# Kernel tuning notes

Hardware: AMD Instinct MI355X
Metric: run time of the kernel (lower is better)

The kernel has to match this reference:

```python
import jax, jax.numpy as jnp
import numpy as np

NEG_SLOPE = 0.01  # nn.LeakyReLU default


def setup_inputs() -> dict:
    key = jax.random.key(0)
    k1, k2, k3, k4, k5, k6 = jax.random.split(key, 6)
    N, E, F_IN, F_OUT = 50000, 800000, 256, 64
    x = jax.random.normal(k1, (N, F_IN), dtype=jnp.float32)
    src = jax.random.randint(k2, (E,), 0, N, dtype=jnp.int32)
    dst = jax.random.randint(k3, (E,), 0, N, dtype=jnp.int32)
    # nn.init.normal_(weight, 0, 0.5) for both Linear layers (no bias)
    W1 = 0.5 * jax.random.normal(k4, (F_OUT, F_IN), dtype=jnp.float32)
    W2 = 0.5 * jax.random.normal(k5, (F_OUT, F_OUT), dtype=jnp.float32)
    # detGAT.a = torch.rand(2*out_feats, 1)
    a = jax.random.uniform(k6, (2 * F_OUT, 1), dtype=jnp.float32)
    return {"x": x, "W1": W1, "W2": W2, "a": a, "src": src, "dst": dst}


def reference(x, W1, W2, a, src, dst):
    N, d = x.shape[0], W1.shape[0]
    # model_base: linear -> (dropout, identity in eval) -> relu, twice
    z = jax.nn.relu(x @ W1.T)
    h = jax.nn.relu(z @ W2.T)  # [N, d]
    # detGAT edge score: LeakyReLU(concat([h_dst, h_src]) @ a)
    # split a so we compute per-node dot products once instead of an [E, 2d] concat
    a_dst, a_src = a[:d, 0], a[d:, 0]
    s_dst = h @ a_dst  # [N]
    s_src = h @ a_src  # [N]
    score = jax.nn.leaky_relu(s_dst[dst] + s_src[src], NEG_SLOPE)  # [E]
    # edge_softmax: softmax over incoming edges of each destination node
    m = jax.ops.segment_max(score, dst, num_segments=N)  # [N]
    e = jnp.exp(score - m[dst])
    ssum = jax.ops.segment_sum(e, dst, num_segments=N)  # [N]
    w = e / ssum[dst]  # [E]
    # weighted scatter-sum of src features to dst nodes
    res = jax.ops.segment_sum(h[src] * w[:, None], dst, num_segments=N)  # [N, d]
    return jax.nn.relu(h - res)
```

## Files before the change

kernel.cpp:

```cpp
#include <hip/hip_runtime.h>
#include <math.h>

#define F_IN 256
#define F_OUT 64
#define NEG_SLOPE 0.01f
#define CAP 8192
#define NB2 256

typedef unsigned short ushort8_t __attribute__((ext_vector_type(8)));
typedef __bf16 bf16x8 __attribute__((ext_vector_type(8)));
typedef float f32x16 __attribute__((ext_vector_type(16)));

__device__ inline unsigned short f2bf(float f) {
    unsigned u = __float_as_uint(f);
    u += 0x7FFF + ((u >> 16) & 1);
    return (unsigned short)(u >> 16);
}
__device__ inline float bf2f(unsigned short u) {
    return __uint_as_float(((unsigned)u) << 16);
}
__device__ inline void splitbf(float x, unsigned short& hi, unsigned short& lo) {
    hi = f2bf(x);
    lo = f2bf(x - bf2f(hi));
}
__device__ inline bf16x8 asbf8(ushort8_t u) {
    union { ushort8_t u; bf16x8 b; } c; c.u = u; return c.b;
}
__device__ inline void split8(const float4& p0, const float4& p1, bf16x8& ah, bf16x8& al) {
    ushort8_t h, l;
    unsigned short th, tl;
    splitbf(p0.x, th, tl); h[0] = th; l[0] = tl;
    splitbf(p0.y, th, tl); h[1] = th; l[1] = tl;
    splitbf(p0.z, th, tl); h[2] = th; l[2] = tl;
    splitbf(p0.w, th, tl); h[3] = th; l[3] = tl;
    splitbf(p1.x, th, tl); h[4] = th; l[4] = tl;
    splitbf(p1.y, th, tl); h[5] = th; l[5] = tl;
    splitbf(p1.z, th, tl); h[6] = th; l[6] = tl;
    splitbf(p1.w, th, tl); h[7] = th; l[7] = tl;
    ah = asbf8(h); al = asbf8(l);
}
__device__ inline float redq32(float v) {
    v += __shfl_xor(v, 1);  v += __shfl_xor(v, 2);  v += __shfl_xor(v, 4);
    v += __shfl_xor(v, 8);  v += __shfl_xor(v, 16);
    return v;
}

__global__ __launch_bounds__(1024)
void prep_scatter_kernel(const float* __restrict__ W1, const float* __restrict__ W2,
                         unsigned short* __restrict__ w1fh, unsigned short* __restrict__ w1fl,
                         unsigned short* __restrict__ w2fh, unsigned short* __restrict__ w2fl,
                         const int* __restrict__ src, const int* __restrict__ dst,
                         int* __restrict__ cursor, int* __restrict__ edata,
                         int E, int chunk)
{
    __shared__ int lh[256], lbase[256], lcur[256];
    const int tid = threadIdx.x;

    if (blockIdx.x < 16) {
        int idx = blockIdx.x * 1024 + tid;
        int jj = idx & 7, l = (idx >> 3) & 63, t = idx >> 9;
        {
            int nt = t & 1, gks = t >> 1;
            int f = nt * 32 + (l & 31);
            int k = gks * 16 + (l >> 5) * 8 + jj;
            unsigned short hi, lo;
            splitbf(W1[f * F_IN + k], hi, lo);
            w1fh[idx] = hi; w1fl[idx] = lo;
        }
        if (idx < 4096) {
            int nt = t & 1, ks = t >> 1;
            int f = nt * 32 + (l & 31);
            int j = ks * 16 + (l >> 5) * 8 + jj;
            unsigned short hi, lo;
            splitbf(W2[f * F_OUT + j], hi, lo);
            w2fh[idx] = hi; w2fl[idx] = lo;
        }
        return;
    }

    const int bid = blockIdx.x - 16;
    if (tid < 256) lh[tid] = 0;
    __syncthreads();
    const int beg = bid * chunk;
    const int end = min(E, beg + chunk);
    for (int i = beg + tid; i < end; i += 1024)
        atomicAdd(&lh[((unsigned)dst[i]) >> 8], 1);
    __syncthreads();
    if (tid < 256) {
        int c = lh[tid];
        lbase[tid] = c ? atomicAdd(&cursor[tid], c) : 0;
        lcur[tid] = 0;
    }
    __syncthreads();
    for (int i = beg + tid; i < end; i += 1024) {
        int d = dst[i];
        int s = src[i];
        int b = ((unsigned)d) >> 8;
        int rk = atomicAdd(&lcur[b], 1);
        edata[b * CAP + lbase[b] + rk] = ((d & 0xFF) << 16) | s;
    }
}

__global__ __launch_bounds__(256)
void mlp_sort_kernel(const float* __restrict__ x,
                     const unsigned short* __restrict__ w1fh,
                     const unsigned short* __restrict__ w1fl,
                     const unsigned short* __restrict__ w2fh,
                     const unsigned short* __restrict__ w2fl,
                     const float* __restrict__ a,
                     unsigned short* __restrict__ hb,
                     float* __restrict__ sdst,
                     float* __restrict__ ssrc, int N,
                     const int* __restrict__ cursor,
                     const int* __restrict__ edata,
                     int* __restrict__ ssorted,
                     int* __restrict__ cnt, int* __restrict__ offs,
                     int MLPB)
{
    __shared__ __align__(16) unsigned short zbuf[4 * 4224];
    __shared__ int hist[256];
    __shared__ int excl[256];

    const int tid = threadIdx.x;
    const int lane = tid & 63;

    if (blockIdx.x < MLPB) {
        const int wid = __builtin_amdgcn_readfirstlane(tid >> 6);
        const int ml = lane & 31;
        const int q = lane >> 5;
        const int node0w = blockIdx.x * 128 + wid * 32;

        unsigned short* zh = zbuf + wid * 4224;
        unsigned short* zl = zh + 2112;

        const int rowc = min(node0w + ml, N - 1);
        const float* __restrict__ xrow = x + (size_t)rowc * F_IN + q * 8;

        f32x16 acc0, acc1;
#pragma unroll
        for (int i = 0; i < 16; i++) { acc0[i] = 0.f; acc1[i] = 0.f; }

        float4 p0 = *(const float4*)(xrow);
        float4 p1 = *(const float4*)(xrow + 4);
        ushort8_t b0h = *(const ushort8_t*)(w1fh + (lane) * 8);
        ushort8_t b0l = *(const ushort8_t*)(w1fl + (lane) * 8);
        ushort8_t b1h = *(const ushort8_t*)(w1fh + (64 + lane) * 8);
        ushort8_t b1l = *(const ushort8_t*)(w1fl + (64 + lane) * 8);

#pragma unroll
        for (int gks = 0; gks < 16; gks++) {
            const int nx = gks < 15 ? gks + 1 : 15;
            float4 q0 = *(const float4*)(xrow + nx * 16);
            float4 q1 = *(const float4*)(xrow + nx * 16 + 4);
            ushort8_t c0h = *(const ushort8_t*)(w1fh + ((nx * 2 + 0) * 64 + lane) * 8);
            ushort8_t c0l = *(const ushort8_t*)(w1fl + ((nx * 2 + 0) * 64 + lane) * 8);
            ushort8_t c1h = *(const ushort8_t*)(w1fh + ((nx * 2 + 1) * 64 + lane) * 8);
            ushort8_t c1l = *(const ushort8_t*)(w1fl + ((nx * 2 + 1) * 64 + lane) * 8);

            bf16x8 ah, al;
            split8(p0, p1, ah, al);
            acc0 = __builtin_amdgcn_mfma_f32_32x32x16_bf16(ah, asbf8(b0h), acc0, 0, 0, 0);
            acc0 = __builtin_amdgcn_mfma_f32_32x32x16_bf16(ah, asbf8(b0l), acc0, 0, 0, 0);
            acc0 = __builtin_amdgcn_mfma_f32_32x32x16_bf16(al, asbf8(b0h), acc0, 0, 0, 0);
            acc1 = __builtin_amdgcn_mfma_f32_32x32x16_bf16(ah, asbf8(b1h), acc1, 0, 0, 0);
            acc1 = __builtin_amdgcn_mfma_f32_32x32x16_bf16(ah, asbf8(b1l), acc1, 0, 0, 0);
            acc1 = __builtin_amdgcn_mfma_f32_32x32x16_bf16(al, asbf8(b1h), acc1, 0, 0, 0);

            p0 = q0; p1 = q1;
            b0h = c0h; b0l = c0l; b1h = c1h; b1l = c1l;
        }

#pragma unroll
        for (int reg = 0; reg < 16; reg++) {
            int nd = (reg & 3) + 8 * (reg >> 2) + 4 * q;
            float z0 = fmaxf(acc0[reg], 0.f);
            float z1 = fmaxf(acc1[reg], 0.f);
            unsigned short h_, l_;
            splitbf(z0, h_, l_);
            zh[nd * 66 + ml] = h_; zl[nd * 66 + ml] = l_;
            splitbf(z1, h_, l_);
            zh[nd * 66 + 32 + ml] = h_; zl[nd * 66 + 32 + ml] = l_;
        }

        f32x16 hacc0, hacc1;
#pragma unroll
        for (int i = 0; i < 16; i++) { hacc0[i] = 0.f; hacc1[i] = 0.f; }
#pragma unroll
        for (int ks = 0; ks < 4; ks++) {
            ushort8_t wh0 = *(const ushort8_t*)(w2fh + ((ks * 2 + 0) * 64 + lane) * 8);
            ushort8_t wl0 = *(const ushort8_t*)(w2fl + ((ks * 2 + 0) * 64 + lane) * 8);
            ushort8_t wh1 = *(const ushort8_t*)(w2fh + ((ks * 2 + 1) * 64 + lane) * 8);
            ushort8_t wl1 = *(const ushort8_t*)(w2fl + ((ks * 2 + 1) * 64 + lane) * 8);
            bf16x8 ah = asbf8(*(const ushort8_t*)(zh + ml * 66 + ks * 16 + q * 8));
            bf16x8 al = asbf8(*(const ushort8_t*)(zl + ml * 66 + ks * 16 + q * 8));
            hacc0 = __builtin_amdgcn_mfma_f32_32x32x16_bf16(ah, asbf8(wh0), hacc0, 0, 0, 0);
            hacc0 = __builtin_amdgcn_mfma_f32_32x32x16_bf16(ah, asbf8(wl0), hacc0, 0, 0, 0);
            hacc0 = __builtin_amdgcn_mfma_f32_32x32x16_bf16(al, asbf8(wh0), hacc0, 0, 0, 0);
            hacc1 = __builtin_amdgcn_mfma_f32_32x32x16_bf16(ah, asbf8(wh1), hacc1, 0, 0, 0);
            hacc1 = __builtin_amdgcn_mfma_f32_32x32x16_bf16(ah, asbf8(wl1), hacc1, 0, 0, 0);
            hacc1 = __builtin_amdgcn_mfma_f32_32x32x16_bf16(al, asbf8(wh1), hacc1, 0, 0, 0);
        }

        const float aD0 = a[ml],            aD1 = a[32 + ml];
        const float aS0 = a[F_OUT + ml],    aS1 = a[F_OUT + 32 + ml];

        float sdv = 0.f, ssv = 0.f;
#pragma unroll
        for (int reg = 0; reg < 16; reg++) {
            int nd = (reg & 3) + 8 * (reg >> 2) + 4 * q;
            float h0 = fmaxf(hacc0[reg], 0.f);
            float h1 = fmaxf(hacc1[reg], 0.f);
            float td = redq32(h0 * aD0 + h1 * aD1);
            float ts = redq32(h0 * aS0 + h1 * aS1);
            if (ml == nd) { sdv = td; ssv = ts; }
            int gn = node0w + nd;
            if (gn < N) {
                hb[(size_t)gn * F_OUT + ml]      = f2bf(h0);
                hb[(size_t)gn * F_OUT + 32 + ml] = f2bf(h1);
            }
        }
        {
            int gn = node0w + ml;
            if ((((ml >> 2) & 1) == q) && gn < N) {
                sdst[gn] = sdv;
                ssrc[gn] = ssv;
            }
        }
        return;
    }

    const int cb = blockIdx.x - MLPB;
    const int base = cb * CAP;
    const int ecnt = cursor[cb];

    hist[tid] = 0;
    __syncthreads();
    for (int i = tid; i < ecnt; i += 256)
        atomicAdd(&hist[((unsigned)edata[base + i]) >> 16], 1);
    __syncthreads();

    if (tid < 64) {
        int v0 = hist[lane * 4], v1 = hist[lane * 4 + 1];
        int v2 = hist[lane * 4 + 2], v3 = hist[lane * 4 + 3];
        int ts = v0 + v1 + v2 + v3;
        int s = ts;
#pragma unroll
        for (int d = 1; d < 64; d <<= 1) {
            int t = __shfl_up(s, d);
            if (lane >= d) s += t;
        }
        int e = s - ts;
        excl[lane * 4] = e;
        excl[lane * 4 + 1] = e + v0;
        excl[lane * 4 + 2] = e + v0 + v1;
        excl[lane * 4 + 3] = e + v0 + v1 + v2;
    }
    __syncthreads();

    {
        int d = cb * 256 + tid;
        if (d < N) {
            cnt[d] = hist[tid];
            offs[d] = base + excl[tid];
        }
    }
    __syncthreads();

    for (int i = tid; i < ecnt; i += 256) {
        int pack = edata[base + i];
        int low = ((unsigned)pack) >> 16;
        int rk = atomicAdd(&excl[low], 1);
        ssorted[base + rk] = pack & 0xFFFF;
    }
}

__global__ __launch_bounds__(256)
void aggregate_kernel(const unsigned short* __restrict__ hb,
                      const float* __restrict__ sdst,
                      const float* __restrict__ ssrc,
                      const int* __restrict__ offs,
                      const int* __restrict__ cnt,
                      const int* __restrict__ ssorted,
                      float* __restrict__ out, int N)
{
    __shared__ float2 ws_sh[4][64];
    const int tid = threadIdx.x;
    const int lane = tid & 63;
    const int wid = tid >> 6;
    const int g = lane >> 4;
    const int li = lane & 15;
    const int d = blockIdx.x * 16 + wid * 4 + g;
    const bool vd = d < N;

    const int off = vd ? offs[d] : 0;
    const int deg = vd ? cnt[d] : 0;
    const float sdd = vd ? sdst[d] : 0.f;

    float M = -INFINITY, S = 0.f;
    float c0 = 0.f, c1 = 0.f, c2 = 0.f, c3 = 0.f;

    for (int cb = 0; cb < deg; cb += 16) {
        int ce = min(16, deg - cb);
        float score = -INFINITY;
        int s = 0;
        if (li < ce) {
            s = ssorted[off + cb + li];
            float sc = sdd + ssrc[s];
            score = sc > 0.f ? sc : NEG_SLOPE * sc;
        }
        float mc = score;
        mc = fmaxf(mc, __shfl_xor(mc, 1));
        mc = fmaxf(mc, __shfl_xor(mc, 2));
        mc = fmaxf(mc, __shfl_xor(mc, 4));
        mc = fmaxf(mc, __shfl_xor(mc, 8));
        float newM = fmaxf(M, mc);
        float scale = __expf(M - newM);
        float w = (li < ce) ? __expf(score - newM) : 0.f;
        ws_sh[wid][lane] = make_float2(w, __int_as_float(s));
        float csum = w;
        csum += __shfl_xor(csum, 1);
        csum += __shfl_xor(csum, 2);
        csum += __shfl_xor(csum, 4);
        csum += __shfl_xor(csum, 8);
        S = S * scale + csum;
        __builtin_amdgcn_wave_barrier();

        float t0 = 0.f, t1 = 0.f, t2 = 0.f, t3 = 0.f;
#pragma unroll
        for (int e = 0; e < 16; e++) {
            float2 tw = ws_sh[wid][g * 16 + e];
            int se = __float_as_int(tw.y);
            ushort4 r = *(const ushort4*)(hb + (((size_t)(unsigned)se) << 6) + li * 4);
            t0 = fmaf(tw.x, bf2f(r.x), t0);
            t1 = fmaf(tw.x, bf2f(r.y), t1);
            t2 = fmaf(tw.x, bf2f(r.z), t2);
            t3 = fmaf(tw.x, bf2f(r.w), t3);
        }
        c0 = c0 * scale + t0;
        c1 = c1 * scale + t1;
        c2 = c2 * scale + t2;
        c3 = c3 * scale + t3;
        __builtin_amdgcn_wave_barrier();
        M = newM;
    }

    if (vd) {
        ushort4 hr = *(const ushort4*)(hb + (((size_t)(unsigned)d) << 6) + li * 4);
        float inv = (S > 0.f) ? 1.f / S : 0.f;
        float r0 = bf2f(hr.x) - c0 * inv;
        float r1 = bf2f(hr.y) - c1 * inv;
        float r2 = bf2f(hr.z) - c2 * inv;
        float r3 = bf2f(hr.w) - c3 * inv;
        float4 o;
        o.x = r0 > 0.f ? r0 : 0.f;
        o.y = r1 > 0.f ? r1 : 0.f;
        o.z = r2 > 0.f ? r2 : 0.f;
        o.w = r3 > 0.f ? r3 : 0.f;
        *(float4*)(out + (size_t)d * F_OUT + li * 4) = o;
    }
}

extern "C" void kernel_launch(void* const* d_in, const int* in_sizes, int n_in,
                              void* d_out, int out_size, void* d_ws,
                              size_t ws_size, hipStream_t stream)
{
    const float* x  = (const float*)d_in[0];
    const float* W1 = (const float*)d_in[1];
    const float* W2 = (const float*)d_in[2];
    const float* a  = (const float*)d_in[3];
    const int* src  = (const int*)d_in[4];
    const int* dst  = (const int*)d_in[5];
    const int N = in_sizes[0] / F_IN;
    const int E = in_sizes[4];

    float* ws = (float*)d_ws;
    float* sdst = ws;
    float* ssrc = sdst + N;
    unsigned short* w1fh = (unsigned short*)(ssrc + N);
    unsigned short* w1fl = w1fh + 16384;
    unsigned short* w2fh = w1fl + 16384;
    unsigned short* w2fl = w2fh + 4096;
    unsigned short* hb = w2fl + 4096;
    int* cnt    = (int*)(hb + (size_t)N * F_OUT);
    int* offs   = cnt + N;
    int* cursor = offs + N;
    int* edata  = cursor + 256;
    int* ssorted = edata + 196 * CAP;

    const int nbc = (N + 255) >> 8;
    const int MLPB = (N + 127) >> 7;
    const int chunk = (E + NB2 - 1) / NB2;

    hipMemsetAsync(cursor, 0, 256 * sizeof(int), stream);
    prep_scatter_kernel<<<16 + NB2, 1024, 0, stream>>>(W1, W2, w1fh, w1fl, w2fh, w2fl,
                                                       src, dst, cursor, edata, E, chunk);
    mlp_sort_kernel<<<MLPB + nbc, 256, 0, stream>>>(x, w1fh, w1fl, w2fh, w2fl, a,
                                                    hb, sdst, ssrc, N,
                                                    cursor, edata, ssorted, cnt, offs,
                                                    MLPB);
    aggregate_kernel<<<(N + 15) / 16, 256, 0, stream>>>(hb, sdst, ssrc, offs, cnt,
                                                        ssorted, (float*)d_out, N);
}
```

Baseline: 146.1 us.

## Pre-split x into MFMA-fragment bf16 hi/lo arrays in prep kernel

Adds blocks to the prep kernel that convert x into bf16 hi/lo pairs laid out in MFMA fragment order. The MLP kernel then loads those fragments directly instead of reading fp32 x and splitting it inline, and it drops the manual software prefetch. It also sets launch_bounds to 2 blocks per CU. The cost is an extra pass that reads x and writes 2 bytes x 2 per element to the workspace, then reads it back, in exchange for less ALU work in the GEMM loop.

```diff
diff --git a/kernel.cpp b/kernel.cpp
--- a/kernel.cpp
+++ b/kernel.cpp
@@ -26,8 +26,7 @@
 __device__ inline bf16x8 asbf8(ushort8_t u) {
     union { ushort8_t u; bf16x8 b; } c; c.u = u; return c.b;
 }
-__device__ inline void split8(const float4& p0, const float4& p1, bf16x8& ah, bf16x8& al) {
-    ushort8_t h, l;
+__device__ inline void split8u(const float4& p0, const float4& p1, ushort8_t& h, ushort8_t& l) {
     unsigned short th, tl;
     splitbf(p0.x, th, tl); h[0] = th; l[0] = tl;
     splitbf(p0.y, th, tl); h[1] = th; l[1] = tl;
@@ -37,7 +36,6 @@
     splitbf(p1.y, th, tl); h[5] = th; l[5] = tl;
     splitbf(p1.z, th, tl); h[6] = th; l[6] = tl;
     splitbf(p1.w, th, tl); h[7] = th; l[7] = tl;
-    ah = asbf8(h); al = asbf8(l);
 }
 __device__ inline float redq32(float v) {
     v += __shfl_xor(v, 1);  v += __shfl_xor(v, 2);  v += __shfl_xor(v, 4);
@@ -49,6 +47,9 @@
 void prep_scatter_kernel(const float* __restrict__ W1, const float* __restrict__ W2,
                          unsigned short* __restrict__ w1fh, unsigned short* __restrict__ w1fl,
                          unsigned short* __restrict__ w2fh, unsigned short* __restrict__ w2fl,
+                         const float* __restrict__ x,
+                         unsigned short* __restrict__ xfh, unsigned short* __restrict__ xfl,
+                         int NTT, int N,
                          const int* __restrict__ src, const int* __restrict__ dst,
                          int* __restrict__ cursor, int* __restrict__ edata,
                          int E, int chunk)
@@ -78,7 +79,23 @@
         return;
     }
 
-    const int bid = blockIdx.x - 16;
+    if (blockIdx.x < 16 + NTT) {
+        const int t = blockIdx.x - 16;
+        const int gks = tid >> 6, lane = tid & 63;
+        const int ml = lane & 31, q = lane >> 5;
+        const int row = min(t * 32 + ml, N - 1);
+        const float* xr = x + (size_t)row * F_IN + gks * 16 + q * 8;
+        float4 p0 = *(const float4*)xr;
+        float4 p1 = *(const float4*)(xr + 4);
+        ushort8_t h, l;
+        split8u(p0, p1, h, l);
+        size_t off = ((size_t)t * 1024 + tid) * 8;
+        *(ushort8_t*)(xfh + off) = h;
+        *(ushort8_t*)(xfl + off) = l;
+        return;
+    }
+
+    const int bid = blockIdx.x - 16 - NTT;
     if (tid < 256) lh[tid] = 0;
     __syncthreads();
     const int beg = bid * chunk;
@@ -101,8 +118,9 @@
     }
 }
 
-__global__ __launch_bounds__(256)
-void mlp_sort_kernel(const float* __restrict__ x,
+__global__ __launch_bounds__(256, 2)
+void mlp_sort_kernel(const unsigned short* __restrict__ xfh,
+                     const unsigned short* __restrict__ xfl,
                      const unsigned short* __restrict__ w1fh,
                      const unsigned short* __restrict__ w1fl,
                      const unsigned short* __restrict__ w2fh,
@@ -129,45 +147,32 @@
         const int ml = lane & 31;
         const int q = lane >> 5;
         const int node0w = blockIdx.x * 128 + wid * 32;
+        const int t = blockIdx.x * 4 + wid;
 
         unsigned short* zh = zbuf + wid * 4224;
         unsigned short* zl = zh + 2112;
 
-        const int rowc = min(node0w + ml, N - 1);
-        const float* __restrict__ xrow = x + (size_t)rowc * F_IN + q * 8;
+        const unsigned short* __restrict__ xbh = xfh + (size_t)t * 8192;
+        const unsigned short* __restrict__ xbl = xfl + (size_t)t * 8192;
 
         f32x16 acc0, acc1;
 #pragma unroll
         for (int i = 0; i < 16; i++) { acc0[i] = 0.f; acc1[i] = 0.f; }
 
-        float4 p0 = *(const float4*)(xrow);
-        float4 p1 = *(const float4*)(xrow + 4);
-        ushort8_t b0h = *(const ushort8_t*)(w1fh + (lane) * 8);
-        ushort8_t b0l = *(const ushort8_t*)(w1fl + (lane) * 8);
-        ushort8_t b1h = *(const ushort8_t*)(w1fh + (64 + lane) * 8);
-        ushort8_t b1l = *(const ushort8_t*)(w1fl + (64 + lane) * 8);
-
 #pragma unroll
         for (int gks = 0; gks < 16; gks++) {
-            const int nx = gks < 15 ? gks + 1 : 15;
-            float4 q0 = *(const float4*)(xrow + nx * 16);
-            float4 q1 = *(const float4*)(xrow + nx * 16 + 4);
-            ushort8_t c0h = *(const ushort8_t*)(w1fh + ((nx * 2 + 0) * 64 + lane) * 8);
-            ushort8_t c0l = *(const ushort8_t*)(w1fl + ((nx * 2 + 0) * 64 + lane) * 8);
-            ushort8_t c1h = *(const ushort8_t*)(w1fh + ((nx * 2 + 1) * 64 + lane) * 8);
-            ushort8_t c1l = *(const ushort8_t*)(w1fl + ((nx * 2 + 1) * 64 + lane) * 8);
-
-            bf16x8 ah, al;
-            split8(p0, p1, ah, al);
-            acc0 = __builtin_amdgcn_mfma_f32_32x32x16_bf16(ah, asbf8(b0h), acc0, 0, 0, 0);
-            acc0 = __builtin_amdgcn_mfma_f32_32x32x16_bf16(ah, asbf8(b0l), acc0, 0, 0, 0);
-            acc0 = __builtin_amdgcn_mfma_f32_32x32x16_bf16(al, asbf8(b0h), acc0, 0, 0, 0);
-            acc1 = __builtin_amdgcn_mfma_f32_32x32x16_bf16(ah, asbf8(b1h), acc1, 0, 0, 0);
-            acc1 = __builtin_amdgcn_mfma_f32_32x32x16_bf16(ah, asbf8(b1l), acc1, 0, 0, 0);
-            acc1 = __builtin_amdgcn_mfma_f32_32x32x16_bf16(al, asbf8(b1h), acc1, 0, 0, 0);
-
-            p0 = q0; p1 = q1;
-            b0h = c0h; b0l = c0l; b1h = c1h; b1l = c1l;
+            bf16x8 ah = asbf8(*(const ushort8_t*)(xbh + gks * 512 + lane * 8));
+            bf16x8 al = asbf8(*(const ushort8_t*)(xbl + gks * 512 + lane * 8));
+            bf16x8 bh0 = asbf8(*(const ushort8_t*)(w1fh + ((gks * 2 + 0) * 64 + lane) * 8));
+            bf16x8 bl0 = asbf8(*(const ushort8_t*)(w1fl + ((gks * 2 + 0) * 64 + lane) * 8));
+            bf16x8 bh1 = asbf8(*(const ushort8_t*)(w1fh + ((gks * 2 + 1) * 64 + lane) * 8));
+            bf16x8 bl1 = asbf8(*(const ushort8_t*)(w1fl + ((gks * 2 + 1) * 64 + lane) * 8));
+            acc0 = __builtin_amdgcn_mfma_f32_32x32x16_bf16(ah, bh0, acc0, 0, 0, 0);
+            acc0 = __builtin_amdgcn_mfma_f32_32x32x16_bf16(ah, bl0, acc0, 0, 0, 0);
+            acc0 = __builtin_amdgcn_mfma_f32_32x32x16_bf16(al, bh0, acc0, 0, 0, 0);
+            acc1 = __builtin_amdgcn_mfma_f32_32x32x16_bf16(ah, bh1, acc1, 0, 0, 0);
+            acc1 = __builtin_amdgcn_mfma_f32_32x32x16_bf16(ah, bl1, acc1, 0, 0, 0);
+            acc1 = __builtin_amdgcn_mfma_f32_32x32x16_bf16(al, bh1, acc1, 0, 0, 0);
         }
 
 #pragma unroll
@@ -187,18 +192,18 @@
         for (int i = 0; i < 16; i++) { hacc0[i] = 0.f; hacc1[i] = 0.f; }
 #pragma unroll
         for (int ks = 0; ks < 4; ks++) {
-            ushort8_t wh0 = *(const ushort8_t*)(w2fh + ((ks * 2 + 0) * 64 + lane) * 8);
-            ushort8_t wl0 = *(const ushort8_t*)(w2fl + ((ks * 2 + 0) * 64 + lane) * 8);
-            ushort8_t wh1 = *(const ushort8_t*)(w2fh + ((ks * 2 + 1) * 64 + lane) * 8);
-            ushort8_t wl1 = *(const ushort8_t*)(w2fl + ((ks * 2 + 1) * 64 + lane) * 8);
+            bf16x8 wh0 = asbf8(*(const ushort8_t*)(w2fh + ((ks * 2 + 0) * 64 + lane) * 8));
+            bf16x8 wl0 = asbf8(*(const ushort8_t*)(w2fl + ((ks * 2 + 0) * 64 + lane) * 8));
+            bf16x8 wh1 = asbf8(*(const ushort8_t*)(w2fh + ((ks * 2 + 1) * 64 + lane) * 8));
+            bf16x8 wl1 = asbf8(*(const ushort8_t*)(w2fl + ((ks * 2 + 1) * 64 + lane) * 8));
             bf16x8 ah = asbf8(*(const ushort8_t*)(zh + ml * 66 + ks * 16 + q * 8));
             bf16x8 al = asbf8(*(const ushort8_t*)(zl + ml * 66 + ks * 16 + q * 8));
-            hacc0 = __builtin_amdgcn_mfma_f32_32x32x16_bf16(ah, asbf8(wh0), hacc0, 0, 0, 0);
-            hacc0 = __builtin_amdgcn_mfma_f32_32x32x16_bf16(ah, asbf8(wl0), hacc0, 0, 0, 0);
-            hacc0 = __builtin_amdgcn_mfma_f32_32x32x16_bf16(al, asbf8(wh0), hacc0, 0, 0, 0);
-            hacc1 = __builtin_amdgcn_mfma_f32_32x32x16_bf16(ah, asbf8(wh1), hacc1, 0, 0, 0);
-            hacc1 = __builtin_amdgcn_mfma_f32_32x32x16_bf16(ah, asbf8(wl1), hacc1, 0, 0, 0);
-            hacc1 = __builtin_amdgcn_mfma_f32_32x32x16_bf16(al, asbf8(wh1), hacc1, 0, 0, 0);
+            hacc0 = __builtin_amdgcn_mfma_f32_32x32x16_bf16(ah, wh0, hacc0, 0, 0, 0);
+            hacc0 = __builtin_amdgcn_mfma_f32_32x32x16_bf16(ah, wl0, hacc0, 0, 0, 0);
+            hacc0 = __builtin_amdgcn_mfma_f32_32x32x16_bf16(al, wh0, hacc0, 0, 0, 0);
+            hacc1 = __builtin_amdgcn_mfma_f32_32x32x16_bf16(ah, wh1, hacc1, 0, 0, 0);
+            hacc1 = __builtin_amdgcn_mfma_f32_32x32x16_bf16(ah, wl1, hacc1, 0, 0, 0);
+            hacc1 = __builtin_amdgcn_mfma_f32_32x32x16_bf16(al, wh1, hacc1, 0, 0, 0);
         }
 
         const float aD0 = a[ml],            aD1 = a[32 + ml];
@@ -373,6 +378,11 @@
     const int N = in_sizes[0] / F_IN;
     const int E = in_sizes[4];
 
+    const int nbc = (N + 255) >> 8;
+    const int MLPB = (N + 127) >> 7;
+    const int NTT = MLPB * 4;
+    const int chunk = (E + NB2 - 1) / NB2;
+
     float* ws = (float*)d_ws;
     float* sdst = ws;
     float* ssrc = sdst + N;
@@ -380,21 +390,21 @@
     unsigned short* w1fl = w1fh + 16384;
     unsigned short* w2fh = w1fl + 16384;
     unsigned short* w2fl = w2fh + 4096;
-    unsigned short* hb = w2fl + 4096;
+    unsigned short* xfh = w2fl + 4096;
+    unsigned short* xfl = xfh + (size_t)NTT * 8192;
+    unsigned short* hb = xfl + (size_t)NTT * 8192;
     int* cnt    = (int*)(hb + (size_t)N * F_OUT);
     int* offs   = cnt + N;
     int* cursor = offs + N;
     int* edata  = cursor + 256;
     int* ssorted = edata + 196 * CAP;
 
-    const int nbc = (N + 255) >> 8;
-    const int MLPB = (N + 127) >> 7;
-    const int chunk = (E + NB2 - 1) / NB2;
-
     hipMemsetAsync(cursor, 0, 256 * sizeof(int), stream);
-    prep_scatter_kernel<<<16 + NB2, 1024, 0, stream>>>(W1, W2, w1fh, w1fl, w2fh, w2fl,
-                                                       src, dst, cursor, edata, E, chunk);
-    mlp_sort_kernel<<<MLPB + nbc, 256, 0, stream>>>(x, w1fh, w1fl, w2fh, w2fl, a,
+    prep_scatter_kernel<<<16 + NTT + NB2, 1024, 0, stream>>>(
+        W1, W2, w1fh, w1fl, w2fh, w2fl,
+        x, xfh, xfl, NTT, N,
+        src, dst, cursor, edata, E, chunk);
+    mlp_sort_kernel<<<MLPB + nbc, 256, 0, stream>>>(xfh, xfl, w1fh, w1fl, w2fh, w2fl, a,
                                                     hb, sdst, ssrc, N,
                                                     cursor, edata, ssorted, cnt, offs,
                                                     MLPB);
```

New measurement: 161.3 us. +10.4%, slower.
